# Kernel optimization log

Measured on AMD Instinct MI355X. Metric: run time of the kernel, lower is better.

Reference implementation:

```python
import jax, jax.numpy as jnp
import numpy as np

B, F_, N, C, H = 32, 2048, 25, 3, 64  # batch, frames, nodes, in_channels, hidden_dim


def setup_inputs() -> dict:
    key = jax.random.key(0)
    k0, k1, k2, k3, k4 = jax.random.split(key, 5)
    x = jax.random.normal(k0, (B, C, F_, N), dtype=jnp.float32)
    mask = jax.random.randint(k1, (N, N), 0, 2).astype(jnp.float32)  # binary adjacency
    # nn.Linear(in_channels, hidden_dim)
    W = jax.random.normal(k2, (C, H), dtype=jnp.float32) / np.sqrt(C).astype(np.float32)
    bW = jnp.zeros((H,), dtype=jnp.float32)
    # nn.Linear(2*hidden_dim, 1) split into the half acting on h_i and the half on h_j
    a1 = jax.random.normal(k3, (H,), dtype=jnp.float32) / np.sqrt(2 * H).astype(np.float32)
    a2 = jax.random.normal(k4, (H,), dtype=jnp.float32) / np.sqrt(2 * H).astype(np.float32)
    ab = jnp.zeros((), dtype=jnp.float32)
    return {"x": x, "mask": mask, "W": W, "bW": bW, "a1": a1, "a2": a2, "ab": ab}


def reference(x, mask, W, bW, a1, a2, ab):
    # x: [B, C, F, N] -> [B, F, N, C]
    xp = jnp.transpose(x, (0, 2, 3, 1))
    h = xp @ W + bW                                  # [B, F, N, H]
    # score[b,f,i,j] = weight([h_i ; h_j]) = a1.h_i + a2.h_j + ab  (concat-linear decomposed)
    s1 = h @ a1                                      # [B, F, N]
    s2 = h @ a2                                      # [B, F, N]
    scores = s1[..., :, None] + s2[..., None, :] + ab  # [B, F, N, N]
    attn = jax.nn.softmax(scores, axis=-1)
    masked = attn * mask                             # broadcast [N,N]
    # torch.einsum('bfnn,bfnj->bfnj') takes the DIAGONAL of masked over its last two axes
    diag = jnp.diagonal(masked, axis1=-2, axis2=-1)  # [B, F, N]
    out = diag[..., None] * h                        # [B, F, N, H]
    return jnp.transpose(out, (0, 3, 1, 2))          # [B, H, F, N]
```

## Files before the change

kernel.cpp:

```cpp
#include <hip/hip_runtime.h>


namespace {
constexpr int B_ = 32, C_ = 3, F_ = 2048, N_ = 25, H_ = 64;
constexpr int TF = 64;
constexpr int TPOS = TF * N_;
constexpr int TVEC = TPOS / 4;
constexpr int FN = F_ * N_;
constexpr int THREADS = 256;
}

__global__ __launch_bounds__(THREADS) void gat_fused(
    const float* __restrict__ x, const float* __restrict__ mask,
    const float* __restrict__ W, const float* __restrict__ bW,
    const float* __restrict__ a2, float* __restrict__ out)
{
  __shared__ float4 x4[3 * TVEC];
  __shared__ float4 d4[TVEC];
  __shared__ float Wl[C_ * H_];
  __shared__ float bWl[H_];
  __shared__ float a2l[H_];
  __shared__ float mdl[N_];
  __shared__ float wal[C_];

  const int tid = threadIdx.x;
  const int blk = blockIdx.x;
  const int b  = blk >> 5;
  const int ft = blk & 31;
  const size_t fbase = (size_t)ft * TPOS;

  if (tid < C_ * H_) Wl[tid] = W[tid];
  if (tid < H_) { bWl[tid] = bW[tid]; a2l[tid] = a2[tid]; }
  if (tid < N_) mdl[tid] = mask[tid * N_ + tid];

  const float4* xg = (const float4*)x;
  for (int i = tid; i < 3 * TVEC; i += THREADS) {
    int c = i / TVEC;
    int j = i - c * TVEC;
    x4[i] = xg[(((size_t)(b * 3 + c) * FN + fbase) >> 2) + j];
  }
  __syncthreads();

  if (tid < C_) {
    float s = 0.f;
    for (int h = 0; h < H_; ++h) s += Wl[tid * H_ + h] * a2l[h];
    wal[tid] = s;
  }
  __syncthreads();

  if (tid < TF) {
    const float* xl = (const float*)x4;
    const float wa0 = wal[0], wa1 = wal[1], wa2 = wal[2];
    const int base = tid * N_;
    float s[N_];
    float m = -3.0e38f;
#pragma unroll
    for (int n = 0; n < N_; ++n) {
      float v = fmaf(xl[2 * TPOS + base + n], wa2,
                fmaf(xl[TPOS + base + n], wa1, xl[base + n] * wa0));
      s[n] = v;
      m = fmaxf(m, v);
    }
    float z = 0.f;
#pragma unroll
    for (int n = 0; n < N_; ++n) { s[n] = __expf(s[n] - m); z += s[n]; }
    const float inv = 1.f / z;
    float* dl = (float*)d4;
#pragma unroll
    for (int n = 0; n < N_; ++n) dl[base + n] = s[n] * inv * mdl[n];
  }
  __syncthreads();

  const bool has2 = (tid + THREADS) < TVEC;
  const float4 xa0 = x4[tid];
  const float4 xa1 = x4[TVEC + tid];
  const float4 xa2 = x4[2 * TVEC + tid];
  const float4 da  = d4[tid];
  float4 xb0 = {}, xb1 = {}, xb2 = {}, db = {};
  if (has2) {
    xb0 = x4[tid + THREADS];
    xb1 = x4[TVEC + tid + THREADS];
    xb2 = x4[2 * TVEC + tid + THREADS];
    db  = d4[tid + THREADS];
  }

  float4* og = (float4*)out;
  const size_t ob = ((size_t)b * H_ * FN + fbase) >> 2;
  for (int h = 0; h < H_; ++h) {
    const float w0 = Wl[h], w1 = Wl[H_ + h], w2 = Wl[2 * H_ + h], bw = bWl[h];
    const size_t vb = ob + (size_t)h * (FN / 4);
    float4 o;
    o.x = da.x * fmaf(xa2.x, w2, fmaf(xa1.x, w1, fmaf(xa0.x, w0, bw)));
    o.y = da.y * fmaf(xa2.y, w2, fmaf(xa1.y, w1, fmaf(xa0.y, w0, bw)));
    o.z = da.z * fmaf(xa2.z, w2, fmaf(xa1.z, w1, fmaf(xa0.z, w0, bw)));
    o.w = da.w * fmaf(xa2.w, w2, fmaf(xa1.w, w1, fmaf(xa0.w, w0, bw)));
    og[vb + tid] = o;
    if (has2) {
      float4 o2;
      o2.x = db.x * fmaf(xb2.x, w2, fmaf(xb1.x, w1, fmaf(xb0.x, w0, bw)));
      o2.y = db.y * fmaf(xb2.y, w2, fmaf(xb1.y, w1, fmaf(xb0.y, w0, bw)));
      o2.z = db.z * fmaf(xb2.z, w2, fmaf(xb1.z, w1, fmaf(xb0.z, w0, bw)));
      o2.w = db.w * fmaf(xb2.w, w2, fmaf(xb1.w, w1, fmaf(xb0.w, w0, bw)));
      og[vb + tid + THREADS] = o2;
    }
  }
}

extern "C" void kernel_launch(void* const* d_in, const int* in_sizes, int n_in,
                              void* d_out, int out_size, void* d_ws, size_t ws_size,
                              hipStream_t stream) {
  const float* x    = (const float*)d_in[0];
  const float* mask = (const float*)d_in[1];
  const float* W    = (const float*)d_in[2];
  const float* bW   = (const float*)d_in[3];
  const float* a2   = (const float*)d_in[5];
  float* out = (float*)d_out;

  dim3 grid(B_ * (F_ / TF));
  dim3 block(THREADS);
  hipLaunchKernelGGL(gat_fused, grid, block, 0, stream, x, mask, W, bW, a2, out);
}
```

Baseline: 88.02 us.

## Split fused kernel into diagonal-softmax pass and wide output-write pass

Splits the single fused kernel into two launches. The first computes the per-position softmax diagonal weight and stores it to workspace. The second runs one thread per float4 position across many more blocks and writes the 64 hidden channels with nontemporal stores. The aim is to fix the low parallelism of the original 1024-block kernel, where only 64 threads did the softmax and each thread then ran the full write loop. The cost is an extra launch, a round trip of the diagonal through global memory, and re-reading x; the old fused kernel stays as a fallback when no workspace is given.

After: 88.94 us. Within noise of the previous version (+1.0%).

```diff
diff --git a/kernel.cpp b/kernel.cpp
--- a/kernel.cpp
+++ b/kernel.cpp
@@ -1,25 +1,26 @@
 #include <hip/hip_runtime.h>
 
+
+typedef float vfloat4 __attribute__((ext_vector_type(4)));
 
 namespace {
 constexpr int B_ = 32, C_ = 3, F_ = 2048, N_ = 25, H_ = 64;
+constexpr int FN = F_ * N_;
+constexpr int FN4 = FN / 4;
 constexpr int TF = 64;
 constexpr int TPOS = TF * N_;
 constexpr int TVEC = TPOS / 4;
-constexpr int FN = F_ * N_;
 constexpr int THREADS = 256;
-}
-
-__global__ __launch_bounds__(THREADS) void gat_fused(
+constexpr size_t D_BYTES = (size_t)B_ * FN * sizeof(float);
+}
+
+__global__ __launch_bounds__(THREADS) void gat_diag(
     const float* __restrict__ x, const float* __restrict__ mask,
-    const float* __restrict__ W, const float* __restrict__ bW,
-    const float* __restrict__ a2, float* __restrict__ out)
+    const float* __restrict__ W, const float* __restrict__ a2,
+    float* __restrict__ dout)
 {
-  __shared__ float4 x4[3 * TVEC];
-  __shared__ float4 d4[TVEC];
-  __shared__ float Wl[C_ * H_];
-  __shared__ float bWl[H_];
-  __shared__ float a2l[H_];
+  __shared__ vfloat4 x4[3 * TVEC];
+  __shared__ vfloat4 d4[TVEC];
   __shared__ float mdl[N_];
   __shared__ float wal[C_];
 
@@ -29,22 +30,19 @@
   const int ft = blk & 31;
   const size_t fbase = (size_t)ft * TPOS;
 
-  if (tid < C_ * H_) Wl[tid] = W[tid];
-  if (tid < H_) { bWl[tid] = bW[tid]; a2l[tid] = a2[tid]; }
   if (tid < N_) mdl[tid] = mask[tid * N_ + tid];
-
-  const float4* xg = (const float4*)x;
+  if (tid >= 64 && tid < 64 + C_) {
+    const int c = tid - 64;
+    float s = 0.f;
+    for (int h = 0; h < H_; ++h) s += W[c * H_ + h] * a2[h];
+    wal[c] = s;
+  }
+
+  const vfloat4* xg = (const vfloat4*)x;
   for (int i = tid; i < 3 * TVEC; i += THREADS) {
     int c = i / TVEC;
     int j = i - c * TVEC;
-    x4[i] = xg[(((size_t)(b * 3 + c) * FN + fbase) >> 2) + j];
-  }
-  __syncthreads();
-
-  if (tid < C_) {
-    float s = 0.f;
-    for (int h = 0; h < H_; ++h) s += Wl[tid * H_ + h] * a2l[h];
-    wal[tid] = s;
+    x4[i] = xg[(size_t)(b * 3 + c) * FN4 + (fbase >> 2) + j];
   }
   __syncthreads();
 
@@ -71,12 +69,115 @@
   }
   __syncthreads();
 
+  vfloat4* dg = (vfloat4*)dout;
+  const size_t db = ((size_t)b * FN + fbase) >> 2;
+  dg[db + tid] = d4[tid];
+  if (tid < TVEC - THREADS) dg[db + THREADS + tid] = d4[THREADS + tid];
+}
+
+__global__ __launch_bounds__(THREADS) void gat_write(
+    const float* __restrict__ x, const float* __restrict__ d,
+    const float* __restrict__ W, const float* __restrict__ bW,
+    float* __restrict__ out)
+{
+  __shared__ float Wl[C_ * H_];
+  __shared__ float bWl[H_];
+  const int tid = threadIdx.x;
+  if (tid < C_ * H_) Wl[tid] = W[tid];
+  if (tid < H_) bWl[tid] = bW[tid];
+  __syncthreads();
+
+  const size_t p = (size_t)blockIdx.x * THREADS + tid;
+  const int b = (int)(p / FN4);
+  const int j = (int)(p - (size_t)b * FN4);
+
+  const vfloat4* xg = (const vfloat4*)x;
+  const vfloat4 x0 = xg[(size_t)(b * 3 + 0) * FN4 + j];
+  const vfloat4 x1 = xg[(size_t)(b * 3 + 1) * FN4 + j];
+  const vfloat4 x2 = xg[(size_t)(b * 3 + 2) * FN4 + j];
+  const vfloat4 dd = ((const vfloat4*)d)[p];
+
+  vfloat4* og = (vfloat4*)out;
+  const size_t ob = (size_t)b * H_ * FN4 + j;
+#pragma unroll 4
+  for (int h = 0; h < H_; ++h) {
+    const float w0 = Wl[h], w1 = Wl[H_ + h], w2 = Wl[2 * H_ + h], bw = bWl[h];
+    vfloat4 o;
+    o.x = dd.x * fmaf(x2.x, w2, fmaf(x1.x, w1, fmaf(x0.x, w0, bw)));
+    o.y = dd.y * fmaf(x2.y, w2, fmaf(x1.y, w1, fmaf(x0.y, w0, bw)));
+    o.z = dd.z * fmaf(x2.z, w2, fmaf(x1.z, w1, fmaf(x0.z, w0, bw)));
+    o.w = dd.w * fmaf(x2.w, w2, fmaf(x1.w, w1, fmaf(x0.w, w0, bw)));
+    __builtin_nontemporal_store(o, &og[ob + (size_t)h * FN4]);
+  }
+}
+
+__global__ __launch_bounds__(THREADS) void gat_fused(
+    const float* __restrict__ x, const float* __restrict__ mask,
+    const float* __restrict__ W, const float* __restrict__ bW,
+    const float* __restrict__ a2, float* __restrict__ out)
+{
+  __shared__ vfloat4 x4[3 * TVEC];
+  __shared__ vfloat4 d4[TVEC];
+  __shared__ float Wl[C_ * H_];
+  __shared__ float bWl[H_];
+  __shared__ float a2l[H_];
+  __shared__ float mdl[N_];
+  __shared__ float wal[C_];
+
+  const int tid = threadIdx.x;
+  const int blk = blockIdx.x;
+  const int b  = blk >> 5;
+  const int ft = blk & 31;
+  const size_t fbase = (size_t)ft * TPOS;
+
+  if (tid < C_ * H_) Wl[tid] = W[tid];
+  if (tid < H_) { bWl[tid] = bW[tid]; a2l[tid] = a2[tid]; }
+  if (tid < N_) mdl[tid] = mask[tid * N_ + tid];
+
+  const vfloat4* xg = (const vfloat4*)x;
+  for (int i = tid; i < 3 * TVEC; i += THREADS) {
+    int c = i / TVEC;
+    int j = i - c * TVEC;
+    x4[i] = xg[(size_t)(b * 3 + c) * FN4 + (fbase >> 2) + j];
+  }
+  __syncthreads();
+
+  if (tid < C_) {
+    float s = 0.f;
+    for (int h = 0; h < H_; ++h) s += Wl[tid * H_ + h] * a2l[h];
+    wal[tid] = s;
+  }
+  __syncthreads();
+
+  if (tid < TF) {
+    const float* xl = (const float*)x4;
+    const float wa0 = wal[0], wa1 = wal[1], wa2 = wal[2];
+    const int base = tid * N_;
+    float s[N_];
+    float m = -3.0e38f;
+#pragma unroll
+    for (int n = 0; n < N_; ++n) {
+      float v = fmaf(xl[2 * TPOS + base + n], wa2,
+                fmaf(xl[TPOS + base + n], wa1, xl[base + n] * wa0));
+      s[n] = v;
+      m = fmaxf(m, v);
+    }
+    float z = 0.f;
+#pragma unroll
+    for (int n = 0; n < N_; ++n) { s[n] = __expf(s[n] - m); z += s[n]; }
+    const float inv = 1.f / z;
+    float* dl = (float*)d4;
+#pragma unroll
+    for (int n = 0; n < N_; ++n) dl[base + n] = s[n] * inv * mdl[n];
+  }
+  __syncthreads();
+
   const bool has2 = (tid + THREADS) < TVEC;
-  const float4 xa0 = x4[tid];
-  const float4 xa1 = x4[TVEC + tid];
-  const float4 xa2 = x4[2 * TVEC + tid];
-  const float4 da  = d4[tid];
-  float4 xb0 = {}, xb1 = {}, xb2 = {}, db = {};
+  const vfloat4 xa0 = x4[tid];
+  const vfloat4 xa1 = x4[TVEC + tid];
+  const vfloat4 xa2 = x4[2 * TVEC + tid];
+  const vfloat4 da  = d4[tid];
+  vfloat4 xb0 = {}, xb1 = {}, xb2 = {}, db = {};
   if (has2) {
     xb0 = x4[tid + THREADS];
     xb1 = x4[TVEC + tid + THREADS];
@@ -84,19 +185,19 @@
     db  = d4[tid + THREADS];
   }
 
-  float4* og = (float4*)out;
+  vfloat4* og = (vfloat4*)out;
   const size_t ob = ((size_t)b * H_ * FN + fbase) >> 2;
   for (int h = 0; h < H_; ++h) {
     const float w0 = Wl[h], w1 = Wl[H_ + h], w2 = Wl[2 * H_ + h], bw = bWl[h];
-    const size_t vb = ob + (size_t)h * (FN / 4);
-    float4 o;
+    const size_t vb = ob + (size_t)h * FN4;
+    vfloat4 o;
     o.x = da.x * fmaf(xa2.x, w2, fmaf(xa1.x, w1, fmaf(xa0.x, w0, bw)));
     o.y = da.y * fmaf(xa2.y, w2, fmaf(xa1.y, w1, fmaf(xa0.y, w0, bw)));
     o.z = da.z * fmaf(xa2.z, w2, fmaf(xa1.z, w1, fmaf(xa0.z, w0, bw)));
     o.w = da.w * fmaf(xa2.w, w2, fmaf(xa1.w, w1, fmaf(xa0.w, w0, bw)));
     og[vb + tid] = o;
     if (has2) {
-      float4 o2;
+      vfloat4 o2;
       o2.x = db.x * fmaf(xb2.x, w2, fmaf(xb1.x, w1, fmaf(xb0.x, w0, bw)));
       o2.y = db.y * fmaf(xb2.y, w2, fmaf(xb1.y, w1, fmaf(xb0.y, w0, bw)));
       o2.z = db.z * fmaf(xb2.z, w2, fmaf(xb1.z, w1, fmaf(xb0.z, w0, bw)));
@@ -116,7 +217,14 @@
   const float* a2   = (const float*)d_in[5];
   float* out = (float*)d_out;
 
-  dim3 grid(B_ * (F_ / TF));
-  dim3 block(THREADS);
-  hipLaunchKernelGGL(gat_fused, grid, block, 0, stream, x, mask, W, bW, a2, out);
-}
+  if (ws_size >= D_BYTES && d_ws != nullptr) {
+    float* d = (float*)d_ws;
+    hipLaunchKernelGGL(gat_diag, dim3(B_ * (F_ / TF)), dim3(THREADS), 0, stream,
+                       x, mask, W, a2, d);
+    hipLaunchKernelGGL(gat_write, dim3(B_ * FN4 / THREADS), dim3(THREADS), 0, stream,
+                       x, d, W, bW, out);
+  } else {
+    hipLaunchKernelGGL(gat_fused, dim3(B_ * (F_ / TF)), dim3(THREADS), 0, stream,
+                       x, mask, W, bW, a2, out);
+  }
+}
```

## Retile work so each thread owns one float4 output, with nontemporal stores

Applied to the files above, without the earlier changes.

Work is now split by a fixed number of float4 output vectors per block (one per thread) instead of 64 frames per block. Each block loads the frame range that covers its positions, plus a small halo aligned to 4, so every thread is busy in the output loop and the second, half-idle pass is gone. W and bW are packed into one vector per h, the two setup barriers are merged into one, and output writes use nontemporal stores to skip cache pollution. The cost is a small redundant halo load per block, extra index arithmetic, and a softmax phase that uses few threads.

After: 81.97 us (median of 2 runs). 6.9% less time.

```diff
diff --git a/kernel.cpp b/kernel.cpp
--- a/kernel.cpp
+++ b/kernel.cpp
@@ -1,63 +1,70 @@
 #include <hip/hip_runtime.h>
 
 
+typedef float vfloat4 __attribute__((ext_vector_type(4)));
+
 namespace {
 constexpr int B_ = 32, C_ = 3, F_ = 2048, N_ = 25, H_ = 64;
-constexpr int TF = 64;
-constexpr int TPOS = TF * N_;
-constexpr int TVEC = TPOS / 4;
-constexpr int FN = F_ * N_;
+constexpr int FN   = F_ * N_;
+constexpr int FN4  = FN / 4;
 constexpr int THREADS = 256;
+constexpr int JB   = FN4 / THREADS;
+constexpr int MAXW = 264;
 }
 
-__global__ __launch_bounds__(THREADS) void gat_fused(
+__global__ __launch_bounds__(THREADS) void gat_fused2(
     const float* __restrict__ x, const float* __restrict__ mask,
     const float* __restrict__ W, const float* __restrict__ bW,
     const float* __restrict__ a2, float* __restrict__ out)
 {
-  __shared__ float4 x4[3 * TVEC];
-  __shared__ float4 d4[TVEC];
-  __shared__ float Wl[C_ * H_];
-  __shared__ float bWl[H_];
-  __shared__ float a2l[H_];
-  __shared__ float mdl[N_];
-  __shared__ float wal[C_];
+  __shared__ float   xl[3][4 * MAXW];
+  __shared__ float   dl[4 * MAXW];
+  __shared__ vfloat4 Wp[H_];
+  __shared__ float   mdl[N_];
+  __shared__ float   wal[C_];
 
   const int tid = threadIdx.x;
   const int blk = blockIdx.x;
-  const int b  = blk >> 5;
-  const int ft = blk & 31;
-  const size_t fbase = (size_t)ft * TPOS;
+  const int b   = blk / JB;
+  const int jb  = blk - b * JB;
+  const int S   = jb * THREADS;
+  const int p0  = S * 4;
+  const int f0  = p0 / N_;
+  const int f1  = (p0 + 4 * THREADS - 1) / N_;
+  const int nf  = f1 - f0 + 1;
+  const int A0  = (f0 * N_) & ~3;
+  int A1 = (f1 * N_ + N_ + 3) & ~3;
+  if (A1 > FN) A1 = FN;
+  const int cnt4 = (A1 - A0) >> 2;
 
-  if (tid < C_ * H_) Wl[tid] = W[tid];
-  if (tid < H_) { bWl[tid] = bW[tid]; a2l[tid] = a2[tid]; }
-  if (tid < N_) mdl[tid] = mask[tid * N_ + tid];
-
-  const float4* xg = (const float4*)x;
-  for (int i = tid; i < 3 * TVEC; i += THREADS) {
-    int c = i / TVEC;
-    int j = i - c * TVEC;
-    x4[i] = xg[(((size_t)(b * 3 + c) * FN + fbase) >> 2) + j];
+  const vfloat4* xg = (const vfloat4*)x;
+#pragma unroll
+  for (int c = 0; c < 3; ++c) {
+    const vfloat4* src = xg + (size_t)(b * 3 + c) * FN4 + (A0 >> 2);
+    vfloat4* dst = (vfloat4*)xl[c];
+    for (int i = tid; i < cnt4; i += THREADS) dst[i] = src[i];
   }
+  if (tid < H_) {
+    vfloat4 w = {W[tid], W[H_ + tid], W[2 * H_ + tid], bW[tid]};
+    Wp[tid] = w;
+  } else if (tid < H_ + C_) {
+    const int c = tid - H_;
+    float s = 0.f;
+    for (int h = 0; h < H_; ++h) s += W[c * H_ + h] * a2[h];
+    wal[c] = s;
+  }
+  if (tid >= 128 && tid < 128 + N_) mdl[tid - 128] = mask[(tid - 128) * (N_ + 1)];
   __syncthreads();
 
-  if (tid < C_) {
-    float s = 0.f;
-    for (int h = 0; h < H_; ++h) s += Wl[tid * H_ + h] * a2l[h];
-    wal[tid] = s;
-  }
-  __syncthreads();
-
-  if (tid < TF) {
-    const float* xl = (const float*)x4;
+  if (tid < nf) {
     const float wa0 = wal[0], wa1 = wal[1], wa2 = wal[2];
-    const int base = tid * N_;
+    const int base = (f0 + tid) * N_ - A0;
     float s[N_];
     float m = -3.0e38f;
 #pragma unroll
     for (int n = 0; n < N_; ++n) {
-      float v = fmaf(xl[2 * TPOS + base + n], wa2,
-                fmaf(xl[TPOS + base + n], wa1, xl[base + n] * wa0));
+      float v = fmaf(xl[2][base + n], wa2,
+                fmaf(xl[1][base + n], wa1, xl[0][base + n] * wa0));
       s[n] = v;
       m = fmaxf(m, v);
     }
@@ -65,44 +72,28 @@
 #pragma unroll
     for (int n = 0; n < N_; ++n) { s[n] = __expf(s[n] - m); z += s[n]; }
     const float inv = 1.f / z;
-    float* dl = (float*)d4;
 #pragma unroll
     for (int n = 0; n < N_; ++n) dl[base + n] = s[n] * inv * mdl[n];
   }
   __syncthreads();
 
-  const bool has2 = (tid + THREADS) < TVEC;
-  const float4 xa0 = x4[tid];
-  const float4 xa1 = x4[TVEC + tid];
-  const float4 xa2 = x4[2 * TVEC + tid];
-  const float4 da  = d4[tid];
-  float4 xb0 = {}, xb1 = {}, xb2 = {}, db = {};
-  if (has2) {
-    xb0 = x4[tid + THREADS];
-    xb1 = x4[TVEC + tid + THREADS];
-    xb2 = x4[2 * TVEC + tid + THREADS];
-    db  = d4[tid + THREADS];
-  }
+  const int li = tid + S - (A0 >> 2);
+  const vfloat4 x0 = ((const vfloat4*)xl[0])[li];
+  const vfloat4 x1 = ((const vfloat4*)xl[1])[li];
+  const vfloat4 x2 = ((const vfloat4*)xl[2])[li];
+  const vfloat4 dd = ((const vfloat4*)dl)[li];
 
-  float4* og = (float4*)out;
-  const size_t ob = ((size_t)b * H_ * FN + fbase) >> 2;
+  vfloat4* og = (vfloat4*)out;
+  const size_t ob = (size_t)b * H_ * FN4 + S + tid;
+#pragma unroll 4
   for (int h = 0; h < H_; ++h) {
-    const float w0 = Wl[h], w1 = Wl[H_ + h], w2 = Wl[2 * H_ + h], bw = bWl[h];
-    const size_t vb = ob + (size_t)h * (FN / 4);
-    float4 o;
-    o.x = da.x * fmaf(xa2.x, w2, fmaf(xa1.x, w1, fmaf(xa0.x, w0, bw)));
-    o.y = da.y * fmaf(xa2.y, w2, fmaf(xa1.y, w1, fmaf(xa0.y, w0, bw)));
-    o.z = da.z * fmaf(xa2.z, w2, fmaf(xa1.z, w1, fmaf(xa0.z, w0, bw)));
-    o.w = da.w * fmaf(xa2.w, w2, fmaf(xa1.w, w1, fmaf(xa0.w, w0, bw)));
-    og[vb + tid] = o;
-    if (has2) {
-      float4 o2;
-      o2.x = db.x * fmaf(xb2.x, w2, fmaf(xb1.x, w1, fmaf(xb0.x, w0, bw)));
-      o2.y = db.y * fmaf(xb2.y, w2, fmaf(xb1.y, w1, fmaf(xb0.y, w0, bw)));
-      o2.z = db.z * fmaf(xb2.z, w2, fmaf(xb1.z, w1, fmaf(xb0.z, w0, bw)));
-      o2.w = db.w * fmaf(xb2.w, w2, fmaf(xb1.w, w1, fmaf(xb0.w, w0, bw)));
-      og[vb + tid + THREADS] = o2;
-    }
+    const vfloat4 wv = Wp[h];
+    vfloat4 o;
+    o.x = dd.x * fmaf(x2.x, wv.z, fmaf(x1.x, wv.y, fmaf(x0.x, wv.x, wv.w)));
+    o.y = dd.y * fmaf(x2.y, wv.z, fmaf(x1.y, wv.y, fmaf(x0.y, wv.x, wv.w)));
+    o.z = dd.z * fmaf(x2.z, wv.z, fmaf(x1.z, wv.y, fmaf(x0.z, wv.x, wv.w)));
+    o.w = dd.w * fmaf(x2.w, wv.z, fmaf(x1.w, wv.y, fmaf(x0.w, wv.x, wv.w)));
+    __builtin_nontemporal_store(o, &og[ob + (size_t)h * FN4]);
   }
 }
 
@@ -116,7 +107,6 @@
   const float* a2   = (const float*)d_in[5];
   float* out = (float*)d_out;
 
-  dim3 grid(B_ * (F_ / TF));
-  dim3 block(THREADS);
-  hipLaunchKernelGGL(gat_fused, grid, block, 0, stream, x, mask, W, bW, a2, out);
+  hipLaunchKernelGGL(gat_fused2, dim3(B_ * JB), dim3(THREADS), 0, stream,
+                     x, mask, W, bW, a2, out);
 }
```
